# Kernel tuning notes

Hardware: AMD Instinct MI355X
Metric: run time of the kernel (lower is better)

Reference implementation:

```python
import jax, jax.numpy as jnp
import numpy as np

DIM = 768
NUM_HEADS = 12
HIDDEN = int(DIM * 4.0)
EPS = 1e-5


def setup_inputs() -> dict:
    key = jax.random.key(0)
    ks = jax.random.split(key, 8)
    s = lambda k, shape, scale=0.02: jax.random.normal(k, shape, dtype=jnp.float32) * scale
    return {
        "x": jax.random.normal(ks[0], (8, 1024, DIM), dtype=jnp.float32),
        "ln1_g": jnp.ones((DIM,), jnp.float32),
        "ln1_b": jnp.zeros((DIM,), jnp.float32),
        "qkv_w": s(ks[1], (DIM, 3 * DIM)),
        "qkv_b": jnp.zeros((3 * DIM,), jnp.float32),
        "proj_w": s(ks[2], (DIM, DIM)),
        "proj_b": jnp.zeros((DIM,), jnp.float32),
        "ln2_g": jnp.ones((DIM,), jnp.float32),
        "ln2_b": jnp.zeros((DIM,), jnp.float32),
        "fc1_w": s(ks[3], (DIM, HIDDEN)),
        "fc1_b": jnp.zeros((HIDDEN,), jnp.float32),
        "fc2_w": s(ks[4], (HIDDEN, DIM)),
        "fc2_b": jnp.zeros((DIM,), jnp.float32),
    }


def layer_norm(x, g, b):
    mu = jnp.mean(x, axis=-1, keepdims=True)
    var = jnp.mean(jnp.square(x - mu), axis=-1, keepdims=True)
    return (x - mu) * jax.lax.rsqrt(var + EPS) * g + b


def reference(x, ln1_g, ln1_b, qkv_w, qkv_b, proj_w, proj_b,
              ln2_g, ln2_b, fc1_w, fc1_b, fc2_w, fc2_b):
    B, N, C = x.shape
    H = NUM_HEADS
    Dh = C // H
    scale = Dh ** -0.5

    # --- Attention (pre-norm) ---
    h = layer_norm(x, ln1_g, ln1_b)
    qkv = h @ qkv_w + qkv_b                       # [B, N, 3C]
    qkv = qkv.reshape(B, N, 3, H, Dh)
    q, k, v = qkv[:, :, 0], qkv[:, :, 1], qkv[:, :, 2]  # [B, N, H, Dh]
    attn = jnp.einsum("bqhd,bkhd->bhqk", q, k) * scale  # [B, H, N, N]
    attn = jax.nn.softmax(attn, axis=-1)
    o = jnp.einsum("bhqk,bkhd->bqhd", attn, v).reshape(B, N, C)
    x = x + (o @ proj_w + proj_b)

    # --- MLP (pre-norm) ---
    h = layer_norm(x, ln2_g, ln2_b)
    h = jax.nn.gelu(h @ fc1_w + fc1_b, approximate=False)  # torch nn.GELU = exact erf
    x = x + (h @ fc2_w + fc2_b)
    return x
```

## Files before the change

kernel.cpp:

```cpp
#include <hip/hip_runtime.h>
#include <hip/hip_bf16.h>
#include <cstdint>

using f32x4   = __attribute__((ext_vector_type(4))) float;
using f32x16  = __attribute__((ext_vector_type(16))) float;
using bf16x8  = __attribute__((ext_vector_type(8))) short;

__device__ inline ushort f2bf(float f) {
    union { float f; uint u; } x; x.f = f;
    uint u = x.u;
    return (ushort)((u + 0x7FFFu + ((u >> 16) & 1u)) >> 16);
}

__device__ inline void gload16(const ushort* g, ushort* lds) {
    __builtin_amdgcn_global_load_lds(
        (const __attribute__((address_space(1))) unsigned int*)g,
        (__attribute__((address_space(3))) unsigned int*)lds, 16, 0, 0);
}

__global__ __launch_bounds__(256) void transpose_cast(const float* __restrict__ w,
                                                      ushort* __restrict__ wt,
                                                      int K, int N) {
    __shared__ float tile[32][33];
    const int bn = blockIdx.x * 32;
    const int bk = blockIdx.y * 32;
    const int tx = threadIdx.x & 31, ty = threadIdx.x >> 5;
#pragma unroll
    for (int i = 0; i < 32; i += 8)
        tile[ty + i][tx] = w[(size_t)(bk + ty + i) * N + bn + tx];
    __syncthreads();
#pragma unroll
    for (int i = 0; i < 32; i += 8)
        wt[(size_t)(bn + ty + i) * K + bk + tx] = f2bf(tile[tx][ty + i]);
}

__global__ __launch_bounds__(256) void ln_bf16(const float* __restrict__ x,
                                               const float* __restrict__ g,
                                               const float* __restrict__ b,
                                               ushort* __restrict__ out) {
    const int row = blockIdx.x;
    const float* xr = x + (size_t)row * 768;
    const int t = threadIdx.x;
    float v0 = xr[t], v1 = xr[t + 256], v2 = xr[t + 512];
    float s  = v0 + v1 + v2;
    float sq = v0 * v0 + v1 * v1 + v2 * v2;
#pragma unroll
    for (int off = 32; off > 0; off >>= 1) {
        s  += __shfl_down(s, off);
        sq += __shfl_down(sq, off);
    }
    __shared__ float sa[4], sb[4];
    const int wv = t >> 6, lane = t & 63;
    if (lane == 0) { sa[wv] = s; sb[wv] = sq; }
    __syncthreads();
    s  = sa[0] + sa[1] + sa[2] + sa[3];
    sq = sb[0] + sb[1] + sb[2] + sb[3];
    const float mu   = s * (1.0f / 768.0f);
    const float var  = sq * (1.0f / 768.0f) - mu * mu;
    const float rstd = rsqrtf(var + 1e-5f);
    ushort* orow = out + (size_t)row * 768;
    orow[t]       = f2bf((v0 - mu) * rstd * g[t]       + b[t]);
    orow[t + 256] = f2bf((v1 - mu) * rstd * g[t + 256] + b[t + 256]);
    orow[t + 512] = f2bf((v2 - mu) * rstd * g[t + 512] + b[t + 512]);
}

template <int EPI, int SWZ>
__global__ __launch_bounds__(256) void gemm_bt(const ushort* __restrict__ A,
                                               const ushort* __restrict__ Bt,
                                               const float* __restrict__ bias,
                                               const float* __restrict__ resid,
                                               void* __restrict__ out,
                                               void* __restrict__ out2,
                                               int M, int N, int K, int gx) {
    __shared__ ushort As[3][128 * 32];
    __shared__ ushort Bs[3][128 * 32];
    int bm, bn;
    if (SWZ) {
        const int bid = blockIdx.x;
        const int x = bid & 7, s = bid >> 3;
        bm = ((s / gx) * 8 + x) * 128;
        bn = (s % gx) * 128;
    } else {
        bm = blockIdx.y * 128;
        bn = blockIdx.x * 128;
    }
    const int t    = threadIdx.x;
    const int lane = t & 63;
    const int w    = t >> 6;
    const int wr   = w >> 1, wc = w & 1;
    const int lr   = lane >> 4, lc = lane & 15;

    const f32x4 fzero = {0.f, 0.f, 0.f, 0.f};
    f32x4 acc[4][4];
#pragma unroll
    for (int ai = 0; ai < 4; ++ai)
#pragma unroll
        for (int bj = 0; bj < 4; ++bj) acc[ai][bj] = fzero;

    const int srow = lane >> 2;
    const int sk8  = (lane & 3) * 8;
    const ushort* Ag0 = A  + (size_t)(bm + w * 16 + srow) * K + sk8;
    const ushort* Ag1 = Ag0 + (size_t)64 * K;
    const ushort* Bg0 = Bt + (size_t)(bn + w * 16 + srow) * K + sk8;
    const ushort* Bg1 = Bg0 + (size_t)64 * K;
    const int lo0 = (w * 16) * 32, lo1 = (64 + w * 16) * 32;

    const int nt = K >> 5;
    auto issue = [&](int tile, int buf) {
        const int kb = tile << 5;
        gload16(Ag0 + kb, &As[buf][lo0]);
        gload16(Ag1 + kb, &As[buf][lo1]);
        gload16(Bg0 + kb, &Bs[buf][lo0]);
        gload16(Bg1 + kb, &Bs[buf][lo1]);
    };
    issue(0, 0);
    if (nt > 1) issue(1, 1);

    for (int tk = 0; tk < nt; ++tk) {
        if (tk + 1 < nt) asm volatile("s_waitcnt vmcnt(4)" ::: "memory");
        else             asm volatile("s_waitcnt vmcnt(0)" ::: "memory");
        __builtin_amdgcn_sched_barrier(0);
        __builtin_amdgcn_s_barrier();
        __builtin_amdgcn_sched_barrier(0);
        if (tk + 2 < nt) issue(tk + 2, (tk + 2) % 3);
        const int cb = tk % 3;
        bf16x8 af[4], bf[4];
#pragma unroll
        for (int ai = 0; ai < 4; ++ai)
            af[ai] = *(const bf16x8*)&As[cb][(wr * 64 + ai * 16 + lc) * 32 + lr * 8];
#pragma unroll
        for (int bj = 0; bj < 4; ++bj)
            bf[bj] = *(const bf16x8*)&Bs[cb][(wc * 64 + bj * 16 + lc) * 32 + lr * 8];
#pragma unroll
        for (int ai = 0; ai < 4; ++ai)
#pragma unroll
            for (int bj = 0; bj < 4; ++bj)
                acc[ai][bj] = __builtin_amdgcn_mfma_f32_16x16x32_bf16(af[ai], bf[bj],
                                                                      acc[ai][bj], 0, 0, 0);
    }

#pragma unroll
    for (int ai = 0; ai < 4; ++ai) {
#pragma unroll
        for (int bj = 0; bj < 4; ++bj) {
            int col  = bn + wc * 64 + bj * 16 + lc;
            float bs = bias[col];
            if (EPI == 3 && col >= 1536) {
                int row0 = bm + wr * 64 + ai * 16 + lr * 4;
                int bb   = row0 >> 10, key0 = row0 & 1023;
                int c    = col - 1536;
                int h    = c >> 6, d = c & 63;
                ushort4 pk;
                pk.x = f2bf(acc[ai][bj][0] + bs);
                pk.y = f2bf(acc[ai][bj][1] + bs);
                pk.z = f2bf(acc[ai][bj][2] + bs);
                pk.w = f2bf(acc[ai][bj][3] + bs);
                *(ushort4*)((ushort*)out2 +
                            ((size_t)(bb * 12 + h) * 64 + d) * 1024 + key0) = pk;
                continue;
            }
            const float qsc = (EPI == 3 && col < 768) ? 0.125f : 1.0f;
#pragma unroll
            for (int j = 0; j < 4; ++j) {
                int row   = bm + wr * 64 + ai * 16 + lr * 4 + j;
                float val = acc[ai][bj][j] + bs;
                if (EPI == 1) {
                    val += resid[(size_t)row * N + col];
                    ((float*)out)[(size_t)row * N + col] = val;
                } else if (EPI == 2) {
                    val = 0.5f * val * (1.0f + erff(val * 0.70710678118f));
                    ((ushort*)out)[(size_t)row * N + col] = f2bf(val);
                } else {
                    ((ushort*)out)[(size_t)row * N + col] = f2bf(val * qsc);
                }
            }
        }
    }
}

__global__ __launch_bounds__(256) void attn_mfma(const ushort* __restrict__ qkv,
                                                 const ushort* __restrict__ vT,
                                                 ushort* __restrict__ outb) {
    __shared__ ushort Kls[64 * 72];
    __shared__ ushort Vtls[64 * 72];

    const int bid = blockIdx.x;
    const int b   = bid / 96;
    const int rem = bid % 96;
    const int h   = rem >> 3;
    const int qc  = rem & 7;
    const int t    = threadIdx.x;
    const int w    = t >> 6;
    const int lane = t & 63;
    const int l31  = lane & 31;
    const int hi   = lane >> 5;
    const int q0   = qc * 128 + w * 32;
    const size_t bbase = (size_t)b * 1024;
    const ushort* vTh = vT + ((size_t)(b * 12 + h) * 64) * 1024;

    bf16x8 qb[4];
    {
        const size_t qrow = (bbase + q0 + l31) * 2304 + h * 64;
#pragma unroll
        for (int dblk = 0; dblk < 4; ++dblk)
            qb[dblk] = *(const bf16x8*)(qkv + qrow + dblk * 16 + hi * 8);
    }

    f32x16 O[2];
#pragma unroll
    for (int ob = 0; ob < 2; ++ob)
#pragma unroll
        for (int r = 0; r < 16; ++r) O[ob][r] = 0.0f;
    float m = -INFINITY, l = 0.0f;

    for (int kt = 0; kt < 16; ++kt) {
        const int k0 = kt * 64;
        __syncthreads();
#pragma unroll
        for (int i = 0; i < 2; ++i) {
            int idx = t + i * 256;
            int key = idx >> 3, seg = idx & 7;
            uint4 u = *(const uint4*)(qkv + (bbase + k0 + key) * 2304 + 768 +
                                      h * 64 + seg * 8);
            *(uint4*)&Kls[key * 72 + seg * 8] = u;
        }
#pragma unroll
        for (int i = 0; i < 2; ++i) {
            int idx = t + i * 256;
            int d = idx >> 3, seg = idx & 7;
            uint4 u = *(const uint4*)(vTh + (size_t)d * 1024 + k0 + seg * 8);
            *(uint4*)&Vtls[d * 72 + seg * 8] = u;
        }
        __syncthreads();

        f32x16 s[2];
#pragma unroll
        for (int kb = 0; kb < 2; ++kb) {
            f32x16 acc;
#pragma unroll
            for (int r = 0; r < 16; ++r) acc[r] = 0.0f;
#pragma unroll
            for (int dblk = 0; dblk < 4; ++dblk) {
                bf16x8 ka = *(const bf16x8*)&Kls[(kb * 32 + l31) * 72 + dblk * 16 + hi * 8];
                acc = __builtin_amdgcn_mfma_f32_32x32x16_bf16(ka, qb[dblk], acc, 0, 0, 0);
            }
            s[kb] = acc;
        }

        float v = s[0][0];
#pragma unroll
        for (int r = 1; r < 16; ++r) v = fmaxf(v, s[0][r]);
#pragma unroll
        for (int r = 0; r < 16; ++r) v = fmaxf(v, s[1][r]);
        v = fmaxf(v, __shfl_xor(v, 32));
        float mn = fmaxf(m, v);
        float c  = __expf(m - mn);
        m = mn;
        float psum = 0.0f;
#pragma unroll
        for (int kb = 0; kb < 2; ++kb)
#pragma unroll
            for (int r = 0; r < 16; ++r) {
                float p = __expf(s[kb][r] - mn);
                s[kb][r] = p;
                psum += p;
            }
        psum += __shfl_xor(psum, 32);
        l = l * c + psum;
#pragma unroll
        for (int ob = 0; ob < 2; ++ob)
#pragma unroll
            for (int r = 0; r < 16; ++r) O[ob][r] *= c;

        bf16x8 pb[4];
#pragma unroll
        for (int kb16 = 0; kb16 < 4; ++kb16) {
            const int sb = kb16 >> 1, r0 = (kb16 & 1) * 8;
            uint own01 = (uint)f2bf(s[sb][r0 + 0]) | ((uint)f2bf(s[sb][r0 + 1]) << 16);
            uint own23 = (uint)f2bf(s[sb][r0 + 2]) | ((uint)f2bf(s[sb][r0 + 3]) << 16);
            uint own45 = (uint)f2bf(s[sb][r0 + 4]) | ((uint)f2bf(s[sb][r0 + 5]) << 16);
            uint own67 = (uint)f2bf(s[sb][r0 + 6]) | ((uint)f2bf(s[sb][r0 + 7]) << 16);
            uint sw01 = __shfl_xor(own01, 32);
            uint sw23 = __shfl_xor(own23, 32);
            uint sw45 = __shfl_xor(own45, 32);
            uint sw67 = __shfl_xor(own67, 32);
            uint d0 = hi ? sw45 : own01;
            uint d1 = hi ? sw67 : own23;
            uint d2 = hi ? own45 : sw01;
            uint d3 = hi ? own67 : sw23;
            union { uint u[4]; bf16x8 v; } cvt;
            cvt.u[0] = d0; cvt.u[1] = d1; cvt.u[2] = d2; cvt.u[3] = d3;
            pb[kb16] = cvt.v;
        }

#pragma unroll
        for (int ob = 0; ob < 2; ++ob)
#pragma unroll
            for (int kb16 = 0; kb16 < 4; ++kb16) {
                bf16x8 va = *(const bf16x8*)&Vtls[(ob * 32 + l31) * 72 + kb16 * 16 + hi * 8];
                O[ob] = __builtin_amdgcn_mfma_f32_32x32x16_bf16(va, pb[kb16], O[ob], 0, 0, 0);
            }
    }

    const float inv = 1.0f / l;
    ushort* orow = outb + (bbase + q0 + l31) * 768 + h * 64;
#pragma unroll
    for (int ob = 0; ob < 2; ++ob)
#pragma unroll
        for (int qd = 0; qd < 4; ++qd) {
            ushort4 pk;
            pk.x = f2bf(O[ob][qd * 4 + 0] * inv);
            pk.y = f2bf(O[ob][qd * 4 + 1] * inv);
            pk.z = f2bf(O[ob][qd * 4 + 2] * inv);
            pk.w = f2bf(O[ob][qd * 4 + 3] * inv);
            *(ushort4*)(orow + ob * 32 + qd * 8 + hi * 4) = pk;
        }
}

extern "C" void kernel_launch(void* const* d_in, const int* in_sizes, int n_in,
                              void* d_out, int out_size, void* d_ws, size_t ws_size,
                              hipStream_t stream) {
    const float* x      = (const float*)d_in[0];
    const float* ln1_g  = (const float*)d_in[1];
    const float* ln1_b  = (const float*)d_in[2];
    const float* qkv_w  = (const float*)d_in[3];
    const float* qkv_b  = (const float*)d_in[4];
    const float* proj_w = (const float*)d_in[5];
    const float* proj_b = (const float*)d_in[6];
    const float* ln2_g  = (const float*)d_in[7];
    const float* ln2_b  = (const float*)d_in[8];
    const float* fc1_w  = (const float*)d_in[9];
    const float* fc1_b  = (const float*)d_in[10];
    const float* fc2_w  = (const float*)d_in[11];
    const float* fc2_b  = (const float*)d_in[12];

    char* ws = (char*)d_ws;
    auto alloc = [&](size_t bytes) {
        char* p = ws;
        ws += (bytes + 255) & ~(size_t)255;
        return p;
    };
    ushort* qkv_wt  = (ushort*)alloc((size_t)768 * 2304 * 2);
    ushort* proj_wt = (ushort*)alloc((size_t)768 * 768 * 2);
    ushort* fc1_wt  = (ushort*)alloc((size_t)768 * 3072 * 2);
    ushort* fc2_wt  = (ushort*)alloc((size_t)3072 * 768 * 2);
    ushort* hb      = (ushort*)alloc((size_t)8192 * 768 * 2);
    ushort* qkvb    = (ushort*)alloc((size_t)8192 * 2304 * 2);
    ushort* vTb     = (ushort*)alloc((size_t)96 * 64 * 1024 * 2);
    ushort* ob      = (ushort*)alloc((size_t)8192 * 768 * 2);
    float*  x1      = (float*)alloc((size_t)8192 * 768 * 4);
    ushort* h2b     = (ushort*)alloc((size_t)8192 * 768 * 2);
    ushort* h3b     = (ushort*)alloc((size_t)8192 * 3072 * 2);

    transpose_cast<<<dim3(2304 / 32, 768 / 32), 256, 0, stream>>>(qkv_w, qkv_wt, 768, 2304);
    transpose_cast<<<dim3(768 / 32, 768 / 32), 256, 0, stream>>>(proj_w, proj_wt, 768, 768);
    transpose_cast<<<dim3(3072 / 32, 768 / 32), 256, 0, stream>>>(fc1_w, fc1_wt, 768, 3072);
    transpose_cast<<<dim3(768 / 32, 3072 / 32), 256, 0, stream>>>(fc2_w, fc2_wt, 3072, 768);

    ln_bf16<<<8192, 256, 0, stream>>>(x, ln1_g, ln1_b, hb);
    gemm_bt<3, 1><<<18 * 64, 256, 0, stream>>>(
        hb, qkv_wt, qkv_b, nullptr, qkvb, vTb, 8192, 2304, 768, 18);
    attn_mfma<<<768, 256, 0, stream>>>(qkvb, vTb, ob);
    gemm_bt<1, 1><<<6 * 64, 256, 0, stream>>>(
        ob, proj_wt, proj_b, x, x1, nullptr, 8192, 768, 768, 6);
    ln_bf16<<<8192, 256, 0, stream>>>(x1, ln2_g, ln2_b, h2b);
    gemm_bt<2, 1><<<24 * 64, 256, 0, stream>>>(
        h2b, fc1_wt, fc1_b, nullptr, h3b, nullptr, 8192, 3072, 768, 24);
    gemm_bt<1, 1><<<6 * 64, 256, 0, stream>>>(
        h3b, fc2_wt, fc2_b, x1, (float*)d_out, nullptr, 8192, 768, 3072, 6);
}
```

Measured before the change: 298.1 us.

## Switch GEMM tiles to 256x64 with one wave per 64-row strip and double buffering

Changes the GEMM block tile from 128x128 to 256x64, so each wave owns a full 64-row strip and reads all 64 B columns. The LDS pipeline drops from triple to double buffering, with a full vmcnt(0) wait before every k-step. This roughly doubles the block count, which may help occupancy and load balance. The costs are a worse A:B reuse ratio (more A traffic per output), less prefetch depth, and exposed load latency.

```diff
diff --git a/kernel.cpp b/kernel.cpp
--- a/kernel.cpp
+++ b/kernel.cpp
@@ -64,7 +64,7 @@
     orow[t + 512] = f2bf((v2 - mu) * rstd * g[t + 512] + b[t + 512]);
 }
 
-template <int EPI, int SWZ>
+template <int EPI>
 __global__ __launch_bounds__(256) void gemm_bt(const ushort* __restrict__ A,
                                                const ushort* __restrict__ Bt,
                                                const float* __restrict__ bias,
@@ -72,22 +72,15 @@
                                                void* __restrict__ out,
                                                void* __restrict__ out2,
                                                int M, int N, int K, int gx) {
-    __shared__ ushort As[3][128 * 32];
-    __shared__ ushort Bs[3][128 * 32];
-    int bm, bn;
-    if (SWZ) {
-        const int bid = blockIdx.x;
-        const int x = bid & 7, s = bid >> 3;
-        bm = ((s / gx) * 8 + x) * 128;
-        bn = (s % gx) * 128;
-    } else {
-        bm = blockIdx.y * 128;
-        bn = blockIdx.x * 128;
-    }
+    __shared__ ushort As[2][256 * 32];
+    __shared__ ushort Bs[2][64 * 32];
+    const int bid = blockIdx.x;
+    const int x = bid & 7, s = bid >> 3;
+    const int bm = ((s / gx) * 8 + x) * 256;
+    const int bn = (s % gx) * 64;
     const int t    = threadIdx.x;
     const int lane = t & 63;
     const int w    = t >> 6;
-    const int wr   = w >> 1, wc = w & 1;
     const int lr   = lane >> 4, lc = lane & 15;
 
     const f32x4 fzero = {0.f, 0.f, 0.f, 0.f};
@@ -99,54 +92,55 @@
 
     const int srow = lane >> 2;
     const int sk8  = (lane & 3) * 8;
-    const ushort* Ag0 = A  + (size_t)(bm + w * 16 + srow) * K + sk8;
-    const ushort* Ag1 = Ag0 + (size_t)64 * K;
-    const ushort* Bg0 = Bt + (size_t)(bn + w * 16 + srow) * K + sk8;
-    const ushort* Bg1 = Bg0 + (size_t)64 * K;
-    const int lo0 = (w * 16) * 32, lo1 = (64 + w * 16) * 32;
+    const ushort* Ag[4];
+#pragma unroll
+    for (int i = 0; i < 4; ++i)
+        Ag[i] = A + (size_t)(bm + (w * 4 + i) * 16 + srow) * K + sk8;
+    const ushort* Bg = Bt + (size_t)(bn + w * 16 + srow) * K + sk8;
+    const int loA = (w * 64) * 32;
+    const int loB = (w * 16) * 32;
 
     const int nt = K >> 5;
     auto issue = [&](int tile, int buf) {
         const int kb = tile << 5;
-        gload16(Ag0 + kb, &As[buf][lo0]);
-        gload16(Ag1 + kb, &As[buf][lo1]);
-        gload16(Bg0 + kb, &Bs[buf][lo0]);
-        gload16(Bg1 + kb, &Bs[buf][lo1]);
+#pragma unroll
+        for (int i = 0; i < 4; ++i)
+            gload16(Ag[i] + kb, &As[buf][loA + i * 512]);
+        gload16(Bg + kb, &Bs[buf][loB]);
     };
     issue(0, 0);
-    if (nt > 1) issue(1, 1);
-
+
+    int cur = 0;
     for (int tk = 0; tk < nt; ++tk) {
-        if (tk + 1 < nt) asm volatile("s_waitcnt vmcnt(4)" ::: "memory");
-        else             asm volatile("s_waitcnt vmcnt(0)" ::: "memory");
+        asm volatile("s_waitcnt vmcnt(0)" ::: "memory");
         __builtin_amdgcn_sched_barrier(0);
         __builtin_amdgcn_s_barrier();
         __builtin_amdgcn_sched_barrier(0);
-        if (tk + 2 < nt) issue(tk + 2, (tk + 2) % 3);
-        const int cb = tk % 3;
+        if (tk + 1 < nt) issue(tk + 1, cur ^ 1);
         bf16x8 af[4], bf[4];
 #pragma unroll
         for (int ai = 0; ai < 4; ++ai)
-            af[ai] = *(const bf16x8*)&As[cb][(wr * 64 + ai * 16 + lc) * 32 + lr * 8];
+            af[ai] = *(const bf16x8*)&As[cur][(w * 64 + ai * 16 + lc) * 32 + lr * 8];
 #pragma unroll
         for (int bj = 0; bj < 4; ++bj)
-            bf[bj] = *(const bf16x8*)&Bs[cb][(wc * 64 + bj * 16 + lc) * 32 + lr * 8];
+            bf[bj] = *(const bf16x8*)&Bs[cur][(bj * 16 + lc) * 32 + lr * 8];
 #pragma unroll
         for (int ai = 0; ai < 4; ++ai)
 #pragma unroll
             for (int bj = 0; bj < 4; ++bj)
                 acc[ai][bj] = __builtin_amdgcn_mfma_f32_16x16x32_bf16(af[ai], bf[bj],
                                                                       acc[ai][bj], 0, 0, 0);
+        cur ^= 1;
     }
 
 #pragma unroll
     for (int ai = 0; ai < 4; ++ai) {
 #pragma unroll
         for (int bj = 0; bj < 4; ++bj) {
-            int col  = bn + wc * 64 + bj * 16 + lc;
+            int col  = bn + bj * 16 + lc;
             float bs = bias[col];
             if (EPI == 3 && col >= 1536) {
-                int row0 = bm + wr * 64 + ai * 16 + lr * 4;
+                int row0 = bm + w * 64 + ai * 16 + lr * 4;
                 int bb   = row0 >> 10, key0 = row0 & 1023;
                 int c    = col - 1536;
                 int h    = c >> 6, d = c & 63;
@@ -162,7 +156,7 @@
             const float qsc = (EPI == 3 && col < 768) ? 0.125f : 1.0f;
 #pragma unroll
             for (int j = 0; j < 4; ++j) {
-                int row   = bm + wr * 64 + ai * 16 + lr * 4 + j;
+                int row   = bm + w * 64 + ai * 16 + lr * 4 + j;
                 float val = acc[ai][bj][j] + bs;
                 if (EPI == 1) {
                     val += resid[(size_t)row * N + col];
@@ -358,14 +352,14 @@
     transpose_cast<<<dim3(768 / 32, 3072 / 32), 256, 0, stream>>>(fc2_w, fc2_wt, 3072, 768);
 
     ln_bf16<<<8192, 256, 0, stream>>>(x, ln1_g, ln1_b, hb);
-    gemm_bt<3, 1><<<18 * 64, 256, 0, stream>>>(
-        hb, qkv_wt, qkv_b, nullptr, qkvb, vTb, 8192, 2304, 768, 18);
+    gemm_bt<3><<<32 * 36, 256, 0, stream>>>(
+        hb, qkv_wt, qkv_b, nullptr, qkvb, vTb, 8192, 2304, 768, 36);
     attn_mfma<<<768, 256, 0, stream>>>(qkvb, vTb, ob);
-    gemm_bt<1, 1><<<6 * 64, 256, 0, stream>>>(
-        ob, proj_wt, proj_b, x, x1, nullptr, 8192, 768, 768, 6);
+    gemm_bt<1><<<32 * 12, 256, 0, stream>>>(
+        ob, proj_wt, proj_b, x, x1, nullptr, 8192, 768, 768, 12);
     ln_bf16<<<8192, 256, 0, stream>>>(x1, ln2_g, ln2_b, h2b);
-    gemm_bt<2, 1><<<24 * 64, 256, 0, stream>>>(
-        h2b, fc1_wt, fc1_b, nullptr, h3b, nullptr, 8192, 3072, 768, 24);
-    gemm_bt<1, 1><<<6 * 64, 256, 0, stream>>>(
-        h3b, fc2_wt, fc2_b, x1, (float*)d_out, nullptr, 8192, 768, 3072, 6);
-}
+    gemm_bt<2><<<32 * 48, 256, 0, stream>>>(
+        h2b, fc1_wt, fc1_b, nullptr, h3b, nullptr, 8192, 3072, 768, 48);
+    gemm_bt<1><<<32 * 12, 256, 0, stream>>>(
+        h3b, fc2_wt, fc2_b, x1, (float*)d_out, nullptr, 8192, 768, 3072, 12);
+}
```

Measured after the change: 326.5 us. 9.5% more time.

## Replace LDS-staged GEMM pipeline with direct global-to-register double buffering

Applied to the files above, without the earlier changes.

The GEMM kernel stops staging A/B tiles through shared memory with global_load_lds and a triple-buffered barrier pipeline. Each wave now loads its own MFMA fragments straight from global memory into registers, ping-ponging two register sets across k-steps. This removes the LDS traffic and the per-iteration block barriers, but each A and B fragment is now read from global memory by two waves instead of once per block. It also raises register pressure and relies on the cache to absorb the redundant reads.

```diff
diff --git a/kernel.cpp b/kernel.cpp
--- a/kernel.cpp
+++ b/kernel.cpp
@@ -10,12 +10,6 @@
     union { float f; uint u; } x; x.f = f;
     uint u = x.u;
     return (ushort)((u + 0x7FFFu + ((u >> 16) & 1u)) >> 16);
-}
-
-__device__ inline void gload16(const ushort* g, ushort* lds) {
-    __builtin_amdgcn_global_load_lds(
-        (const __attribute__((address_space(1))) unsigned int*)g,
-        (__attribute__((address_space(3))) unsigned int*)lds, 16, 0, 0);
 }
 
 __global__ __launch_bounds__(256) void transpose_cast(const float* __restrict__ w,
@@ -64,7 +58,7 @@
     orow[t + 512] = f2bf((v2 - mu) * rstd * g[t + 512] + b[t + 512]);
 }
 
-template <int EPI, int SWZ>
+template <int EPI>
 __global__ __launch_bounds__(256) void gemm_bt(const ushort* __restrict__ A,
                                                const ushort* __restrict__ Bt,
                                                const float* __restrict__ bias,
@@ -72,18 +66,10 @@
                                                void* __restrict__ out,
                                                void* __restrict__ out2,
                                                int M, int N, int K, int gx) {
-    __shared__ ushort As[3][128 * 32];
-    __shared__ ushort Bs[3][128 * 32];
-    int bm, bn;
-    if (SWZ) {
-        const int bid = blockIdx.x;
-        const int x = bid & 7, s = bid >> 3;
-        bm = ((s / gx) * 8 + x) * 128;
-        bn = (s % gx) * 128;
-    } else {
-        bm = blockIdx.y * 128;
-        bn = blockIdx.x * 128;
-    }
+    const int bid = blockIdx.x;
+    const int x = bid & 7, s = bid >> 3;
+    const int bm = ((s / gx) * 8 + x) * 128;
+    const int bn = (s % gx) * 128;
     const int t    = threadIdx.x;
     const int lane = t & 63;
     const int w    = t >> 6;
@@ -97,45 +83,45 @@
 #pragma unroll
         for (int bj = 0; bj < 4; ++bj) acc[ai][bj] = fzero;
 
-    const int srow = lane >> 2;
-    const int sk8  = (lane & 3) * 8;
-    const ushort* Ag0 = A  + (size_t)(bm + w * 16 + srow) * K + sk8;
-    const ushort* Ag1 = Ag0 + (size_t)64 * K;
-    const ushort* Bg0 = Bt + (size_t)(bn + w * 16 + srow) * K + sk8;
-    const ushort* Bg1 = Bg0 + (size_t)64 * K;
-    const int lo0 = (w * 16) * 32, lo1 = (64 + w * 16) * 32;
-
+    const ushort* pa[4];
+    const ushort* pb[4];
+#pragma unroll
+    for (int i = 0; i < 4; ++i) {
+        pa[i] = A  + (size_t)(bm + wr * 64 + i * 16 + lc) * K + lr * 8;
+        pb[i] = Bt + (size_t)(bn + wc * 64 + i * 16 + lc) * K + lr * 8;
+    }
+
+    bf16x8 a0[4], b0[4], a1[4], b1[4];
     const int nt = K >> 5;
-    auto issue = [&](int tile, int buf) {
-        const int kb = tile << 5;
-        gload16(Ag0 + kb, &As[buf][lo0]);
-        gload16(Ag1 + kb, &As[buf][lo1]);
-        gload16(Bg0 + kb, &Bs[buf][lo0]);
-        gload16(Bg1 + kb, &Bs[buf][lo1]);
-    };
-    issue(0, 0);
-    if (nt > 1) issue(1, 1);
-
-    for (int tk = 0; tk < nt; ++tk) {
-        if (tk + 1 < nt) asm volatile("s_waitcnt vmcnt(4)" ::: "memory");
-        else             asm volatile("s_waitcnt vmcnt(0)" ::: "memory");
-        __builtin_amdgcn_sched_barrier(0);
-        __builtin_amdgcn_s_barrier();
-        __builtin_amdgcn_sched_barrier(0);
-        if (tk + 2 < nt) issue(tk + 2, (tk + 2) % 3);
-        const int cb = tk % 3;
-        bf16x8 af[4], bf[4];
+#pragma unroll
+    for (int i = 0; i < 4; ++i) { a0[i] = *(const bf16x8*)(pa[i]); }
+#pragma unroll
+    for (int i = 0; i < 4; ++i) { b0[i] = *(const bf16x8*)(pb[i]); }
+
+    for (int tk = 0; tk < nt; tk += 2) {
+        const int k1 = (tk + 1) << 5;
+#pragma unroll
+        for (int i = 0; i < 4; ++i) { a1[i] = *(const bf16x8*)(pa[i] + k1); }
+#pragma unroll
+        for (int i = 0; i < 4; ++i) { b1[i] = *(const bf16x8*)(pb[i] + k1); }
 #pragma unroll
         for (int ai = 0; ai < 4; ++ai)
-            af[ai] = *(const bf16x8*)&As[cb][(wr * 64 + ai * 16 + lc) * 32 + lr * 8];
-#pragma unroll
-        for (int bj = 0; bj < 4; ++bj)
-            bf[bj] = *(const bf16x8*)&Bs[cb][(wc * 64 + bj * 16 + lc) * 32 + lr * 8];
+#pragma unroll
+            for (int bj = 0; bj < 4; ++bj)
+                acc[ai][bj] = __builtin_amdgcn_mfma_f32_16x16x32_bf16(a0[ai], b0[bj],
+                                                                      acc[ai][bj], 0, 0, 0);
+        if (tk + 2 < nt) {
+            const int k2 = (tk + 2) << 5;
+#pragma unroll
+            for (int i = 0; i < 4; ++i) { a0[i] = *(const bf16x8*)(pa[i] + k2); }
+#pragma unroll
+            for (int i = 0; i < 4; ++i) { b0[i] = *(const bf16x8*)(pb[i] + k2); }
+        }
 #pragma unroll
         for (int ai = 0; ai < 4; ++ai)
 #pragma unroll
             for (int bj = 0; bj < 4; ++bj)
-                acc[ai][bj] = __builtin_amdgcn_mfma_f32_16x16x32_bf16(af[ai], bf[bj],
+                acc[ai][bj] = __builtin_amdgcn_mfma_f32_16x16x32_bf16(a1[ai], b1[bj],
                                                                       acc[ai][bj], 0, 0, 0);
     }
 
@@ -358,14 +344,14 @@
     transpose_cast<<<dim3(768 / 32, 3072 / 32), 256, 0, stream>>>(fc2_w, fc2_wt, 3072, 768);
 
     ln_bf16<<<8192, 256, 0, stream>>>(x, ln1_g, ln1_b, hb);
-    gemm_bt<3, 1><<<18 * 64, 256, 0, stream>>>(
+    gemm_bt<3><<<18 * 64, 256, 0, stream>>>(
         hb, qkv_wt, qkv_b, nullptr, qkvb, vTb, 8192, 2304, 768, 18);
     attn_mfma<<<768, 256, 0, stream>>>(qkvb, vTb, ob);
-    gemm_bt<1, 1><<<6 * 64, 256, 0, stream>>>(
+    gemm_bt<1><<<6 * 64, 256, 0, stream>>>(
         ob, proj_wt, proj_b, x, x1, nullptr, 8192, 768, 768, 6);
     ln_bf16<<<8192, 256, 0, stream>>>(x1, ln2_g, ln2_b, h2b);
-    gemm_bt<2, 1><<<24 * 64, 256, 0, stream>>>(
+    gemm_bt<2><<<24 * 64, 256, 0, stream>>>(
         h2b, fc1_wt, fc1_b, nullptr, h3b, nullptr, 8192, 3072, 768, 24);
-    gemm_bt<1, 1><<<6 * 64, 256, 0, stream>>>(
+    gemm_bt<1><<<6 * 64, 256, 0, stream>>>(
         h3b, fc2_wt, fc2_b, x1, (float*)d_out, nullptr, 8192, 768, 3072, 6);
 }
```

Result: slower. 566.1 us (+89.9%).
